# Optimization experiments

Measured on AMD Instinct MI355X. Metric: run time of the kernel, lower is better.

The kernel has to match this reference:

```python
import jax, jax.numpy as jnp
import numpy as np

N_HEAD, N_KV_HEAD, HEAD_DIM = 16, 4, 128
EPS = 1e-5


def rms_norm(x, eps=EPS):
    return x * jax.lax.rsqrt(jnp.mean(x * x, axis=-1, keepdims=True) + eps)


def apply_rope(x, cos, sin):
    # x: (B,T,H,D); cos/sin: (1,T,1,D//2)
    d = x.shape[-1] // 2
    x1, x2 = x[..., :d], x[..., d:]
    return jnp.concatenate([x1 * cos - x2 * sin, x1 * sin + x2 * cos], axis=-1)


def setup_inputs() -> dict:
    key = jax.random.key(0)
    ks = jax.random.split(key, 6)
    B, T, C = 4, 2048, 2048
    H, KV, D = N_HEAD, N_KV_HEAD, HEAD_DIM
    x = jax.random.normal(ks[0], (B, T, C), dtype=jnp.float32)
    # RoPE tables (llama-style, theta=10000)
    inv_freq = 1.0 / (10000.0 ** (jnp.arange(D // 2, dtype=jnp.float32) / (D // 2)))
    ang = jnp.arange(T, dtype=jnp.float32)[:, None] * inv_freq[None, :]  # (T, D/2)
    cos = jnp.cos(ang)[None, :, None, :]
    sin = jnp.sin(ang)[None, :, None, :]
    s = 0.02
    wq = jax.random.normal(ks[1], (C, H * D), dtype=jnp.float32) * s
    wk = jax.random.normal(ks[2], (C, KV * D), dtype=jnp.float32) * s
    wv = jax.random.normal(ks[3], (C, KV * D), dtype=jnp.float32) * s
    wproj = jax.random.normal(ks[4], (H * D, C), dtype=jnp.float32) * s
    return {"x": x, "cos": cos, "sin": sin, "wq": wq, "wk": wk, "wv": wv, "wproj": wproj}


def reference(x, cos, sin, wq, wk, wv, wproj):
    B, T, C = x.shape
    H, KV, D = N_HEAD, N_KV_HEAD, HEAD_DIM
    n_rep = H // KV
    q = (x @ wq).reshape(B, T, H, D)
    k = (x @ wk).reshape(B, T, KV, D)
    v = (x @ wv).reshape(B, T, KV, D)
    q = apply_rope(q, cos, sin)
    k = apply_rope(k, cos, sin)
    # QK-norm (use_qk_norm=True)
    q = rms_norm(q)
    k = rms_norm(k)
    # GQA: expand kv heads (matches torch repeat_interleave on head dim)
    k = jnp.repeat(k, n_rep, axis=2)
    v = jnp.repeat(v, n_rep, axis=2)
    scale = 1.0 / np.sqrt(D).astype(np.float32)
    scores = jnp.einsum('bqhd,bkhd->bhqk', q, k) * scale  # (B,H,T,T)
    causal = jnp.tril(jnp.ones((T, T), dtype=bool))
    scores = jnp.where(causal[None, None], scores, jnp.finfo(scores.dtype).min)
    p = jax.nn.softmax(scores, axis=-1)
    y = jnp.einsum('bhqk,bkhd->bqhd', p, v).reshape(B, T, H * D)
    return y @ wproj
```

## Files before the change

### kernel.cpp

```cpp
#include <hip/hip_runtime.h>
#include <hip/hip_bf16.h>
#include <stdint.h>

using bf16 = __hip_bfloat16;
typedef __attribute__((ext_vector_type(8))) short short8;
typedef __attribute__((ext_vector_type(4))) float f32x4;
typedef __attribute__((ext_vector_type(16))) float f32x16;

#define MFMA16(a,b,c) __builtin_amdgcn_mfma_f32_16x16x32_bf16(a,b,c,0,0,0)
#define MFMA32(a,b,c) __builtin_amdgcn_mfma_f32_32x32x16_bf16(a,b,c,0,0,0)

__device__ __forceinline__ void gload_lds16(const void* g, void* l) {
  __builtin_amdgcn_global_load_lds((const __attribute__((address_space(1))) void*)g,
                                   (__attribute__((address_space(3))) void*)l, 16, 0, 0);
}

__device__ __forceinline__ short bf_bits(float f) {
  bf16 h = __float2bfloat16(f);
  return *reinterpret_cast<short*>(&h);
}
__device__ __forceinline__ unsigned int pk2(float a, float b) {
  unsigned int r;
  asm("v_cvt_pk_bf16_f32 %0, %1, %2" : "=v"(r) : "v"(a), "v"(b));
  return r;
}
__device__ __forceinline__ float bf2f(short s) {
  return __uint_as_float((unsigned int)(unsigned short)s << 16);
}
__device__ __forceinline__ float exp2g(float x) { return __builtin_amdgcn_exp2f(x); }

__global__ __launch_bounds__(256) void f32_to_bf16_k(const float* __restrict__ in,
                                                     bf16* __restrict__ out, size_t n) {
  size_t i = ((size_t)blockIdx.x * 256 + threadIdx.x) * 8;
  if (i >= n) return;
  float4 a = *(const float4*)(in + i);
  float4 b = *(const float4*)(in + i + 4);
  short8 pk;
  pk[0] = bf_bits(a.x); pk[1] = bf_bits(a.y); pk[2] = bf_bits(a.z); pk[3] = bf_bits(a.w);
  pk[4] = bf_bits(b.x); pk[5] = bf_bits(b.y); pk[6] = bf_bits(b.z); pk[7] = bf_bits(b.w);
  *(short8*)(out + i) = pk;
}

__global__ __launch_bounds__(256) void transpose_cvt_k(const float* __restrict__ in,
                                                       bf16* __restrict__ out, int K, int N) {
  __shared__ float tile[32][33];
  int n0 = blockIdx.x * 32, k0 = blockIdx.y * 32;
  int tx = threadIdx.x & 31, ty = threadIdx.x >> 5;
#pragma unroll
  for (int j = 0; j < 4; ++j) {
    int kk = ty + j * 8;
    tile[kk][tx] = in[(size_t)(k0 + kk) * N + n0 + tx];
  }
  __syncthreads();
#pragma unroll
  for (int j = 0; j < 4; ++j) {
    int nn = ty + j * 8;
    out[(size_t)(n0 + nn) * K + k0 + tx] = __float2bfloat16(tile[tx][nn]);
  }
}

__global__ __launch_bounds__(256) void transpose_v_k(const bf16* __restrict__ qkv,
                                                     bf16* __restrict__ vt) {
  constexpr int T = 2048, Dh = 128, KV = 4, QKVW = 3072, VOFF = 2560;
  __shared__ bf16 tile[32][33];
  int t0 = blockIdx.x * 32, d0 = blockIdx.y * 32;
  int b = blockIdx.z >> 2, kv = blockIdx.z & 3;
  int tx = threadIdx.x & 31, ty = threadIdx.x >> 5;
#pragma unroll
  for (int j = 0; j < 4; ++j) {
    int tt = ty + j * 8;
    tile[tt][tx] = qkv[((size_t)(b * T + t0 + tt)) * QKVW + VOFF + kv * Dh + d0 + tx];
  }
  __syncthreads();
#pragma unroll
  for (int j = 0; j < 4; ++j) {
    int dd = ty + j * 8;
    vt[((size_t)((b * KV + kv) * Dh + d0 + dd)) * T + t0 + tx] = tile[tx][dd];
  }
}

__global__ __launch_bounds__(256) void rope_rms_k(bf16* __restrict__ buf, int rowstride,
                                                  int baseoff,
                                                  const float* __restrict__ cosp,
                                                  const float* __restrict__ sinp,
                                                  int nh, float outscale) {
  constexpr int T = 2048;
  int wid = blockIdx.x * 4 + (threadIdx.x >> 6);
  int lane = threadIdx.x & 63;
  int h = wid % nh;
  int tok = wid / nh;
  int t = tok & (T - 1);
  bf16* p = buf + (size_t)tok * rowstride + baseoff + h * 128;
  float x1 = __bfloat162float(p[lane]);
  float x2 = __bfloat162float(p[lane + 64]);
  float c = cosp[t * 64 + lane], s = sinp[t * 64 + lane];
  float o1 = x1 * c - x2 * s;
  float o2 = x1 * s + x2 * c;
  float ss = o1 * o1 + o2 * o2;
#pragma unroll
  for (int m = 1; m < 64; m <<= 1) ss += __shfl_xor(ss, m, 64);
  float r = rsqrtf(ss * (1.f / 128.f) + 1e-5f) * outscale;
  p[lane] = __float2bfloat16(o1 * r);
  p[lane + 64] = __float2bfloat16(o2 * r);
}

#define PHASE(buf, i0, ...)                                                       \
  {                                                                               \
    short8 a00 = ldA(buf, i0, 0), a01 = ldA(buf, i0, 1);                          \
    short8 a10 = ldA(buf, (i0) + 1, 0), a11 = ldA(buf, (i0) + 1, 1);              \
    __VA_ARGS__;                                                                  \
    __builtin_amdgcn_s_barrier();                                                 \
    asm volatile("s_waitcnt lgkmcnt(0)" ::: "memory");                            \
    __builtin_amdgcn_s_setprio(1);                                                \
    _Pragma("unroll") for (int j = 0; j < 4; ++j) {                               \
      acc[i0][j] = MFMA16(a00, bf_[2 * j], acc[i0][j]);                           \
      acc[i0][j] = MFMA16(a01, bf_[2 * j + 1], acc[i0][j]);                       \
      acc[(i0) + 1][j] = MFMA16(a10, bf_[2 * j], acc[(i0) + 1][j]);               \
      acc[(i0) + 1][j] = MFMA16(a11, bf_[2 * j + 1], acc[(i0) + 1][j]);           \
    }                                                                             \
    __builtin_amdgcn_s_setprio(0);                                                \
  }
#define LOADB(buf)                                                                \
  _Pragma("unroll") for (int j = 0; j < 4; ++j) {                                 \
    bf_[2 * j] = ldB(buf, j, 0);                                                  \
    bf_[2 * j + 1] = ldB(buf, j, 1);                                              \
  }
#define BAR __builtin_amdgcn_s_barrier()

template <typename OutT>
__global__ __launch_bounds__(512, 2) void gemm256(const bf16* __restrict__ A,
                                                  const bf16* __restrict__ Bt,
                                                  OutT* __restrict__ C, int K,
                                                  int NT, int ldC) {
  __shared__ char lds[131072];
  const int tid = threadIdx.x, lane = tid & 63, w = tid >> 6;
  const int wm = w >> 2, wn = w & 3;
  const int bx = blockIdx.x;
  const int chunk = gridDim.x >> 3;
  const int wgid = (bx & 7) * chunk + (bx >> 3);
  const int m0 = (wgid / NT) * 256, n0 = (wgid % NT) * 256;
  const int lm = lane & 15;
  const int sw = (lane & 7) << 4;
  const int g16 = (lane >> 4) << 4;
  const size_t strideAB = (size_t)K * 2;

  auto stageA = [&](int buf, int h, int t) {
#pragma unroll
    for (int p2 = 0; p2 < 2; ++p2) {
      int off = tid * 16 + p2 * 8192;
      int row = off >> 7, cb = off & 127;
      int scb = cb ^ ((row & 7) << 4);
      gload_lds16((const char*)A + (size_t)(m0 + h * 128 + row) * strideAB + t * 128 + scb,
                  lds + buf * 65536 + h * 16384 + off);
    }
  };
  auto stageB = [&](int buf, int h, int t) {
#pragma unroll
    for (int p2 = 0; p2 < 2; ++p2) {
      int off = tid * 16 + p2 * 8192;
      int row = off >> 7, cb = off & 127;
      int scb = cb ^ ((row & 7) << 4);
      gload_lds16((const char*)Bt + (size_t)(n0 + h * 128 + row) * strideAB + t * 128 + scb,
                  lds + buf * 65536 + 32768 + h * 16384 + off);
    }
  };
  auto ldA = [&](int buf, int i, int ks) {
    int row = wm * 128 + i * 16 + lm;
    return *(const short8*)(lds + buf * 65536 + row * 128 + ((ks * 64 + g16) ^ sw));
  };
  auto ldB = [&](int buf, int j, int ks) {
    int row = wn * 64 + j * 16 + lm;
    return *(const short8*)(lds + buf * 65536 + 32768 + row * 128 + ((ks * 64 + g16) ^ sw));
  };

  f32x4 acc[8][4] = {};
  short8 bf_[8];
  const int niter = K / 128;

  stageA(0, 0, 0); stageA(0, 1, 0); stageB(0, 0, 0); stageB(0, 1, 0);
  stageB(1, 0, 1); stageB(1, 1, 1);
  asm volatile("s_waitcnt vmcnt(4)" ::: "memory");
  BAR;

  for (int i = 0; i < niter; ++i) {
    const int t0 = 2 * i, t1 = 2 * i + 1;
    const bool nl = (i + 1 < niter);
    LOADB(0);
    PHASE(0, 0, stageA(1, 0, t1)); BAR;
    PHASE(0, 2, stageA(1, 1, t1)); BAR;
    PHASE(0, 4, if (nl) stageB(0, 0, t0 + 2)); BAR;
    PHASE(0, 6, if (nl) stageB(0, 1, t0 + 2));
    if (nl) { asm volatile("s_waitcnt vmcnt(4)" ::: "memory"); }
    else    { asm volatile("s_waitcnt vmcnt(0)" ::: "memory"); }
    BAR;
    LOADB(1);
    PHASE(1, 0, if (nl) stageA(0, 0, t0 + 2)); BAR;
    PHASE(1, 2, if (nl) stageA(0, 1, t0 + 2)); BAR;
    PHASE(1, 4, if (nl) stageB(1, 0, t1 + 2)); BAR;
    PHASE(1, 6, if (nl) stageB(1, 1, t1 + 2));
    if (nl) { asm volatile("s_waitcnt vmcnt(4)" ::: "memory"); }
    BAR;
  }

  if constexpr (sizeof(OutT) == 2) {
    __syncthreads();
    bf16* sC = (bf16*)lds;
#pragma unroll
    for (int i = 0; i < 8; ++i) {
      int row = wm * 128 + i * 16 + (lane >> 4) * 4;
#pragma unroll
      for (int j = 0; j < 4; ++j) {
        int col = wn * 64 + j * 16 + lm;
#pragma unroll
        for (int r = 0; r < 4; ++r) sC[(row + r) * 256 + col] = __float2bfloat16(acc[i][j][r]);
      }
    }
    __syncthreads();
#pragma unroll
    for (int p = 0; p < 16; ++p) {
      int off = tid * 16 + p * 8192;
      int row = off >> 9, cb = off & 511;
      *(short8*)((char*)C + ((size_t)(m0 + row) * ldC + n0) * 2 + cb) =
          *(const short8*)(lds + off);
    }
  } else {
#pragma unroll
    for (int i = 0; i < 8; ++i) {
      int row = m0 + wm * 128 + i * 16 + (lane >> 4) * 4;
#pragma unroll
      for (int j = 0; j < 4; ++j) {
        int col = n0 + wn * 64 + j * 16 + lm;
#pragma unroll
        for (int r = 0; r < 4; ++r) C[(size_t)(row + r) * ldC + col] = acc[i][j][r];
      }
    }
  }
}

template <typename OutT>
__global__ __launch_bounds__(256) void gemm_bt(const bf16* __restrict__ A,
                                               const bf16* __restrict__ Bt,
                                               OutT* __restrict__ C, int K,
                                               int NT, int ldC) {
  constexpr int BM = 128, BN = 128, BK = 64;
  __shared__ char smem[32768];
  bf16* sA = (bf16*)smem;
  bf16* sB = (bf16*)(smem + 16384);
  int tid = threadIdx.x;
  int lane = tid & 63, w = tid >> 6;
  int flat = blockIdx.x;
  int wgid = (flat & 7) * (gridDim.x >> 3) + (flat >> 3);
  int m0 = (wgid / NT) * BM, n0 = (wgid % NT) * BN;
  int wm = (w >> 1) * 64, wn = (w & 1) * 64;
  f32x4 acc[4][4] = {};
  int nk = K / BK;
  for (int kt = 0; kt < nk; ++kt) {
    __syncthreads();
    int kb = kt * BK;
#pragma unroll
    for (int it = 0; it < 4; ++it) {
      int off = tid * 16 + it * 4096;
      int row = off >> 7, cb = off & 127;
      gload_lds16((const char*)A + (((size_t)(m0 + row)) * K + kb) * 2 + cb, (char*)sA + off);
    }
#pragma unroll
    for (int it = 0; it < 4; ++it) {
      int off = tid * 16 + it * 4096;
      int row = off >> 7, cb = off & 127;
      gload_lds16((const char*)Bt + (((size_t)(n0 + row)) * K + kb) * 2 + cb, (char*)sB + off);
    }
    asm volatile("s_waitcnt vmcnt(0)" ::: "memory");
    __syncthreads();
#pragma unroll
    for (int ks = 0; ks < 2; ++ks) {
      short8 af[4], bfr[4];
#pragma unroll
      for (int i = 0; i < 4; ++i) {
        af[i]  = *(const short8*)(sA + (wm + i * 16 + (lane & 15)) * BK + ks * 32 + (lane >> 4) * 8);
        bfr[i] = *(const short8*)(sB + (wn + i * 16 + (lane & 15)) * BK + ks * 32 + (lane >> 4) * 8);
      }
#pragma unroll
      for (int i = 0; i < 4; ++i)
#pragma unroll
        for (int j = 0; j < 4; ++j)
          acc[i][j] = MFMA16(af[i], bfr[j], acc[i][j]);
    }
  }
  if constexpr (sizeof(OutT) == 2) {
    __syncthreads();
    bf16* sC = (bf16*)smem;
#pragma unroll
    for (int i = 0; i < 4; ++i) {
      int row = wm + i * 16 + (lane >> 4) * 4;
#pragma unroll
      for (int j = 0; j < 4; ++j) {
        int col = wn + j * 16 + (lane & 15);
#pragma unroll
        for (int r = 0; r < 4; ++r)
          sC[(row + r) * BN + col] = __float2bfloat16(acc[i][j][r]);
      }
    }
    __syncthreads();
#pragma unroll
    for (int it = 0; it < 8; ++it) {
      int off = tid * 16 + it * 4096;
      int row = off >> 8, cb = off & 255;
      *(short8*)((char*)C + ((size_t)(m0 + row) * ldC + n0) * 2 + cb) =
          *(const short8*)(smem + off);
    }
  } else {
#pragma unroll
    for (int i = 0; i < 4; ++i) {
      int row = m0 + wm + i * 16 + (lane >> 4) * 4;
#pragma unroll
      for (int j = 0; j < 4; ++j) {
        int col = n0 + wn + j * 16 + (lane & 15);
#pragma unroll
        for (int r = 0; r < 4; ++r)
          C[(size_t)(row + r) * ldC + col] = acc[i][j][r];
      }
    }
  }
}

__global__ __launch_bounds__(512, 2) void attn_k(const bf16* __restrict__ qkv,
                                                 const bf16* __restrict__ vt,
                                                 bf16* __restrict__ y,
                                                 const float* __restrict__ cosp,
                                                 const float* __restrict__ sinp) {
  constexpr int T = 2048, Dh = 128, KV = 4, KB = 64, QKVW = 3072, KOFF = 2048;
  __shared__ char lds[65536];
  const int tid = threadIdx.x, lane = tid & 63, w = tid >> 6;
  const int hi = lane >> 5, lq = lane & 31;
  const int bx = blockIdx.x;
  const int qt = 7 - (bx >> 6);
  const int b = (bx >> 4) & 3, h = bx & 15;
  const int kh = h >> 2;
  const int q0 = qt * 256 + w * 32;
  const int qg = q0 + lq;
  const int swz = (lane & 7) << 4;

  short8 aq[8];
  {
    const bf16* qp = qkv + ((size_t)(b * T + qg)) * QKVW + h * Dh + hi * 8;
#pragma unroll
    for (int m = 0; m < 8; ++m) aq[m] = *(const short8*)(qp + m * 16);
  }
  __builtin_amdgcn_s_waitcnt(0);

  {
    float ss = 0.f;
#pragma unroll
    for (int m = 0; m < 8; ++m)
#pragma unroll
      for (int e = 0; e < 8; ++e) { float v = bf2f(aq[m][e]); ss += v * v; }
    ss += __shfl_xor(ss, 32, 64);
    float rn = rsqrtf(ss * (1.f / 128.f) + 1e-5f) * (0.08838834764831845f * 1.4426950408889634f);
    const float4* cq4 = (const float4*)(cosp + (size_t)qg * 64) + hi * 2;
    const float4* sq4 = (const float4*)(sinp + (size_t)qg * 64) + hi * 2;
#pragma unroll
    for (int m = 0; m < 4; ++m) {
      float4 c0 = cq4[m * 4], c1 = cq4[m * 4 + 1];
      float4 s0 = sq4[m * 4], s1 = sq4[m * 4 + 1];
      float cc[8] = {c0.x, c0.y, c0.z, c0.w, c1.x, c1.y, c1.z, c1.w};
      float sn[8] = {s0.x, s0.y, s0.z, s0.w, s1.x, s1.y, s1.z, s1.w};
      short8 xl = aq[m], xh = aq[m + 4], nl, nh;
#pragma unroll
      for (int e = 0; e < 8; ++e) {
        float x1 = bf2f(xl[e]), x2 = bf2f(xh[e]);
        nl[e] = bf_bits((x1 * cc[e] - x2 * sn[e]) * rn);
        nh[e] = bf_bits((x1 * sn[e] + x2 * cc[e]) * rn);
      }
      aq[m] = nl; aq[m + 4] = nh;
    }
  }

  f32x16 acc[4] = {};
  float mrow = -1e4f, lrow = 0.f;

  auto stage = [&](int buf, int kv0) {
#pragma unroll
    for (int p = 0; p < 2; ++p) {
      int off = tid * 16 + p * 8192;
      int row = off >> 8, cb = off & 255;
      int scb = cb ^ ((row & 7) << 4);
      gload_lds16((const char*)qkv + (((size_t)(b * T + kv0 + row)) * QKVW + KOFF + kh * Dh) * 2 + scb,
                  lds + buf * 16384 + off);
    }
#pragma unroll
    for (int p = 0; p < 2; ++p) {
      int off = tid * 16 + p * 8192;
      int row = off >> 7, cb = off & 127;
      int scb = cb ^ ((row & 7) << 4);
      gload_lds16((const char*)vt + (((size_t)((b * KV + kh) * Dh + row)) * T + kv0) * 2 + scb,
                  lds + 32768 + buf * 16384 + off);
    }
  };

  const int nt = (qt + 1) * 4;
  const int lastit = (q0 + 31) >> 6;
  stage(0, 0);

  for (int it = 0; it < nt; ++it) {
    int cur = it & 1;
    if (it + 1 < nt) { stage(cur ^ 1, (it + 1) * KB); asm volatile("s_waitcnt vmcnt(4)" ::: "memory"); }
    else             { asm volatile("s_waitcnt vmcnt(0)" ::: "memory"); }
    __builtin_amdgcn_s_barrier();
    if (it <= lastit) {
      const char* sK = lds + cur * 16384;
      const char* sV = lds + 32768 + cur * 16384;
      const int kv0 = it * KB;

      f32x16 s0 = {}, s1 = {};
      __builtin_amdgcn_s_setprio(1);
#pragma unroll
      for (int m = 0; m < 8; ++m) {
        short8 ak = *(const short8*)(sK + lq * 256 + ((m * 32 + hi * 16) ^ swz));
        s0 = MFMA32(ak, aq[m], s0);
      }
#pragma unroll
      for (int m = 0; m < 8; ++m) {
        short8 ak = *(const short8*)(sK + (32 + lq) * 256 + ((m * 32 + hi * 16) ^ swz));
        s1 = MFMA32(ak, aq[m], s1);
      }
      __builtin_amdgcn_s_setprio(0);

      if (kv0 + 63 > q0) {
#pragma unroll
        for (int r = 0; r < 16; ++r) {
          int krow = (r & 3) + 8 * (r >> 2) + 4 * hi;
          if (kv0 + krow > qg) s0[r] = -1e30f;
          if (kv0 + 32 + krow > qg) s1[r] = -1e30f;
        }
      }

      float mx[16];
#pragma unroll
      for (int r = 0; r < 16; ++r) mx[r] = fmaxf(s0[r], s1[r]);
#pragma unroll
      for (int st = 8; st > 0; st >>= 1)
#pragma unroll
        for (int r = 0; r < 16; ++r) if (r < st) mx[r] = fmaxf(mx[r], mx[r + st]);
      float tmax = fmaxf(mx[0], __shfl_xor(mx[0], 32, 64));
      if (!__all(tmax - mrow <= 11.5f)) {
        float mn = fmaxf(mrow, tmax);
        float corr = exp2g(mrow - mn);
        mrow = mn;
        lrow *= corr;
#pragma unroll
        for (int dt = 0; dt < 4; ++dt)
#pragma unroll
          for (int r = 0; r < 16; ++r) acc[dt][r] *= corr;
      }
      float sm[16];
#pragma unroll
      for (int r = 0; r < 16; ++r) {
        s0[r] = exp2g(s0[r] - mrow);
        s1[r] = exp2g(s1[r] - mrow);
        sm[r] = s0[r] + s1[r];
      }
#pragma unroll
      for (int st = 8; st > 0; st >>= 1)
#pragma unroll
        for (int r = 0; r < 16; ++r) if (r < st) sm[r] += sm[r + st];
      lrow += sm[0] + __shfl_xor(sm[0], 32, 64);

      unsigned int u[16];
#pragma unroll
      for (int g = 0; g < 4; ++g) {
        u[g * 2 + 0] = pk2(s0[4 * g + 0], s0[4 * g + 1]);
        u[g * 2 + 1] = pk2(s0[4 * g + 2], s0[4 * g + 3]);
        u[8 + g * 2 + 0] = pk2(s1[4 * g + 0], s1[4 * g + 1]);
        u[8 + g * 2 + 1] = pk2(s1[4 * g + 2], s1[4 * g + 3]);
      }
      short8 pb[4];
#pragma unroll
      for (int kvs = 0; kvs < 4; ++kvs) {
        unsigned int lo0 = u[4 * kvs + 0], lo1 = u[4 * kvs + 1];
        unsigned int hi0 = u[4 * kvs + 2], hi1 = u[4 * kvs + 3];
        asm volatile("v_permlane32_swap_b32 %0, %1" : "+v"(lo0), "+v"(hi0));
        asm volatile("v_permlane32_swap_b32 %0, %1" : "+v"(lo1), "+v"(hi1));
        union { short8 v; unsigned int q[4]; } P;
        P.q[0] = lo0; P.q[1] = lo1; P.q[2] = hi0; P.q[3] = hi1;
        pb[kvs] = P.v;
      }

      __builtin_amdgcn_s_setprio(1);
#pragma unroll
      for (int dt = 0; dt < 4; ++dt) {
#pragma unroll
        for (int kvs = 0; kvs < 4; ++kvs) {
          short8 av = *(const short8*)(sV + (dt * 32 + lq) * 128 + ((kvs * 32 + hi * 16) ^ swz));
          acc[dt] = MFMA32(av, pb[kvs], acc[dt]);
        }
      }
      __builtin_amdgcn_s_setprio(0);
    }
    __builtin_amdgcn_s_barrier();
  }

  float inv = 1.f / lrow;
  __syncthreads();
  char* myO = lds + w * 8192;
#pragma unroll
  for (int dt = 0; dt < 4; ++dt)
#pragma unroll
    for (int i = 0; i < 8; ++i) {
      int d = ((2 * i) & 3) + 8 * (i >> 1) + 4 * hi;
      unsigned int pkd = pk2(acc[dt][2 * i] * inv, acc[dt][2 * i + 1] * inv);
      *(unsigned int*)(myO + lq * 256 + ((dt * 64 + d * 2) ^ ((lq & 7) << 4))) = pkd;
    }
  __syncthreads();
  const int row0 = b * T + qt * 256;
#pragma unroll
  for (int p = 0; p < 8; ++p) {
    int off = (p * 512 + tid) * 16;
    int q = off >> 8, cb = off & 255;
    short8 v = *(const short8*)(lds + (q >> 5) * 8192 + (q & 31) * 256 + (cb ^ ((q & 7) << 4)));
    *(short8*)((char*)y + ((size_t)(row0 + q) * 2048 + h * 128) * 2 + cb) = v;
  }
}

extern "C" void kernel_launch(void* const* d_in, const int* in_sizes, int n_in,
                              void* d_out, int out_size, void* d_ws, size_t ws_size,
                              hipStream_t stream) {
  const float* x    = (const float*)d_in[0];
  const float* cosp = (const float*)d_in[1];
  const float* sinp = (const float*)d_in[2];
  const float* wq   = (const float*)d_in[3];
  const float* wk   = (const float*)d_in[4];
  const float* wv   = (const float*)d_in[5];
  const float* wp   = (const float*)d_in[6];
  float* out = (float*)d_out;

  constexpr size_t Mtok = 8192;
  constexpr int Cdim = 2048, HD = 2048, KVD = 512, QKVW = 3072;

  char* ws = (char*)d_ws;
  bf16* xb    = (bf16*)ws; ws += Mtok * Cdim * 2;
  bf16* wqkvT = (bf16*)ws; ws += (size_t)QKVW * Cdim * 2;
  bf16* wpT   = (bf16*)ws; ws += (size_t)Cdim * HD * 2;
  bf16* qkv   = (bf16*)ws; ws += Mtok * QKVW * 2;
  bf16* vtb   = (bf16*)ws; ws += Mtok * KVD * 2;
  bf16* yb    = (bf16*)ws; ws += Mtok * HD * 2;

  f32_to_bf16_k<<<dim3(Mtok * Cdim / 8 / 256), 256, 0, stream>>>(x, xb, Mtok * Cdim);
  transpose_cvt_k<<<dim3(HD / 32, Cdim / 32), 256, 0, stream>>>(wq, wqkvT, Cdim, HD);
  transpose_cvt_k<<<dim3(KVD / 32, Cdim / 32), 256, 0, stream>>>(wk, wqkvT + (size_t)2048 * Cdim, Cdim, KVD);
  transpose_cvt_k<<<dim3(KVD / 32, Cdim / 32), 256, 0, stream>>>(wv, wqkvT + (size_t)2560 * Cdim, Cdim, KVD);
  transpose_cvt_k<<<dim3(Cdim / 32, HD / 32), 256, 0, stream>>>(wp, wpT, HD, Cdim);

  gemm256<bf16><<<dim3(256), 512, 0, stream>>>(xb, wqkvT, qkv, Cdim, 8, QKVW);
  gemm_bt<bf16><<<dim3(512), 256, 0, stream>>>(xb, wqkvT + (size_t)2048 * Cdim,
                                               (bf16*)qkv + 2048, Cdim, 8, QKVW);

  rope_rms_k<<<dim3(Mtok * 4 / 4), 256, 0, stream>>>(qkv, QKVW, 2048, cosp, sinp, 4, 1.0f);
  transpose_v_k<<<dim3(64, 4, 16), 256, 0, stream>>>(qkv, vtb);

  attn_k<<<dim3(512), 512, 0, stream>>>(qkv, vtb, yb, cosp, sinp);

  gemm256<float><<<dim3(256), 512, 0, stream>>>(yb, wpT, out, Cdim, 8, 2048);
}
```

Measured before the change: 316.0 us.

## Fuse K RoPE/RMS-norm and V transpose into KV GEMM epilogue; restructure attention prefetch

The KV projection GEMM becomes a dedicated kernel whose epilogue applies RoPE and RMS-norm to the K tiles in LDS and writes V tiles transposed straight into the vtb buffer. This removes the separate rope_rms_k and transpose_v_k launches and their global memory round trips. Separately, the attention loop now waits for all loads and then issues the next-tile prefetch after the barrier, dropping the trailing barrier. That trades the partial vmcnt wait for a simpler double-buffer schedule, which may expose more load latency.

```diff
diff --git a/kernel.cpp b/kernel.cpp
--- a/kernel.cpp
+++ b/kernel.cpp
@@ -57,51 +57,6 @@
     int nn = ty + j * 8;
     out[(size_t)(n0 + nn) * K + k0 + tx] = __float2bfloat16(tile[tx][nn]);
   }
-}
-
-__global__ __launch_bounds__(256) void transpose_v_k(const bf16* __restrict__ qkv,
-                                                     bf16* __restrict__ vt) {
-  constexpr int T = 2048, Dh = 128, KV = 4, QKVW = 3072, VOFF = 2560;
-  __shared__ bf16 tile[32][33];
-  int t0 = blockIdx.x * 32, d0 = blockIdx.y * 32;
-  int b = blockIdx.z >> 2, kv = blockIdx.z & 3;
-  int tx = threadIdx.x & 31, ty = threadIdx.x >> 5;
-#pragma unroll
-  for (int j = 0; j < 4; ++j) {
-    int tt = ty + j * 8;
-    tile[tt][tx] = qkv[((size_t)(b * T + t0 + tt)) * QKVW + VOFF + kv * Dh + d0 + tx];
-  }
-  __syncthreads();
-#pragma unroll
-  for (int j = 0; j < 4; ++j) {
-    int dd = ty + j * 8;
-    vt[((size_t)((b * KV + kv) * Dh + d0 + dd)) * T + t0 + tx] = tile[tx][dd];
-  }
-}
-
-__global__ __launch_bounds__(256) void rope_rms_k(bf16* __restrict__ buf, int rowstride,
-                                                  int baseoff,
-                                                  const float* __restrict__ cosp,
-                                                  const float* __restrict__ sinp,
-                                                  int nh, float outscale) {
-  constexpr int T = 2048;
-  int wid = blockIdx.x * 4 + (threadIdx.x >> 6);
-  int lane = threadIdx.x & 63;
-  int h = wid % nh;
-  int tok = wid / nh;
-  int t = tok & (T - 1);
-  bf16* p = buf + (size_t)tok * rowstride + baseoff + h * 128;
-  float x1 = __bfloat162float(p[lane]);
-  float x2 = __bfloat162float(p[lane + 64]);
-  float c = cosp[t * 64 + lane], s = sinp[t * 64 + lane];
-  float o1 = x1 * c - x2 * s;
-  float o2 = x1 * s + x2 * c;
-  float ss = o1 * o1 + o2 * o2;
-#pragma unroll
-  for (int m = 1; m < 64; m <<= 1) ss += __shfl_xor(ss, m, 64);
-  float r = rsqrtf(ss * (1.f / 128.f) + 1e-5f) * outscale;
-  p[lane] = __float2bfloat16(o1 * r);
-  p[lane + 64] = __float2bfloat16(o2 * r);
 }
 
 #define PHASE(buf, i0, ...)                                                       \
@@ -237,24 +192,24 @@
   }
 }
 
-template <typename OutT>
-__global__ __launch_bounds__(256) void gemm_bt(const bf16* __restrict__ A,
+__global__ __launch_bounds__(256) void gemm_kv(const bf16* __restrict__ A,
                                                const bf16* __restrict__ Bt,
-                                               OutT* __restrict__ C, int K,
-                                               int NT, int ldC) {
-  constexpr int BM = 128, BN = 128, BK = 64;
-  __shared__ char smem[32768];
+                                               bf16* __restrict__ qkv,
+                                               bf16* __restrict__ vtb,
+                                               const float* __restrict__ cosp,
+                                               const float* __restrict__ sinp) {
+  constexpr int BM = 128, BN = 128, BK = 64, K = 2048, QKVW = 3072, T = 2048, SCP = 132;
+  __shared__ char smem[BM * SCP * 2];
   bf16* sA = (bf16*)smem;
   bf16* sB = (bf16*)(smem + 16384);
   int tid = threadIdx.x;
   int lane = tid & 63, w = tid >> 6;
   int flat = blockIdx.x;
   int wgid = (flat & 7) * (gridDim.x >> 3) + (flat >> 3);
-  int m0 = (wgid / NT) * BM, n0 = (wgid % NT) * BN;
+  int m0 = (wgid >> 3) * BM, n0 = (wgid & 7) * BN;
   int wm = (w >> 1) * 64, wn = (w & 1) * 64;
   f32x4 acc[4][4] = {};
-  int nk = K / BK;
-  for (int kt = 0; kt < nk; ++kt) {
+  for (int kt = 0; kt < K / BK; ++kt) {
     __syncthreads();
     int kb = kt * BK;
 #pragma unroll
@@ -286,9 +241,12 @@
           acc[i][j] = MFMA16(af[i], bfr[j], acc[i][j]);
     }
   }
-  if constexpr (sizeof(OutT) == 2) {
-    __syncthreads();
-    bf16* sC = (bf16*)smem;
+
+  const int kvh = (n0 >> 7) & 3;
+  const int b = m0 >> 11, t0 = m0 & (T - 1);
+  bf16* sC = (bf16*)smem;
+  __syncthreads();
+  if (n0 >= 512) {
 #pragma unroll
     for (int i = 0; i < 4; ++i) {
       int row = wm + i * 16 + (lane >> 4) * 4;
@@ -296,29 +254,51 @@
       for (int j = 0; j < 4; ++j) {
         int col = wn + j * 16 + (lane & 15);
 #pragma unroll
-        for (int r = 0; r < 4; ++r)
-          sC[(row + r) * BN + col] = __float2bfloat16(acc[i][j][r]);
-      }
-    }
-    __syncthreads();
-#pragma unroll
-    for (int it = 0; it < 8; ++it) {
-      int off = tid * 16 + it * 4096;
-      int row = off >> 8, cb = off & 255;
-      *(short8*)((char*)C + ((size_t)(m0 + row) * ldC + n0) * 2 + cb) =
-          *(const short8*)(smem + off);
+        for (int r = 0; r < 4; ++r) sC[col * SCP + row + r] = __float2bfloat16(acc[i][j][r]);
+      }
+    }
+    __syncthreads();
+#pragma unroll
+    for (int p = 0; p < 8; ++p) {
+      int g = p * 2048 + tid * 8;
+      int d = g >> 7, tb = g & 127;
+      *(short8*)(vtb + ((size_t)((b * 4 + kvh) * 128 + d)) * T + t0 + tb) =
+          *(const short8*)(sC + d * SCP + tb);
     }
   } else {
 #pragma unroll
     for (int i = 0; i < 4; ++i) {
-      int row = m0 + wm + i * 16 + (lane >> 4) * 4;
+      int row = wm + i * 16 + (lane >> 4) * 4;
 #pragma unroll
       for (int j = 0; j < 4; ++j) {
-        int col = n0 + wn + j * 16 + (lane & 15);
-#pragma unroll
-        for (int r = 0; r < 4; ++r)
-          C[(size_t)(row + r) * ldC + col] = acc[i][j][r];
-      }
+        int col = wn + j * 16 + (lane & 15);
+#pragma unroll
+        for (int r = 0; r < 4; ++r) sC[(row + r) * SCP + col] = __float2bfloat16(acc[i][j][r]);
+      }
+    }
+    __syncthreads();
+    for (int rr = 0; rr < 32; ++rr) {
+      int row = w * 32 + rr;
+      int t = t0 + row;
+      float x1 = __bfloat162float(sC[row * SCP + lane]);
+      float x2 = __bfloat162float(sC[row * SCP + lane + 64]);
+      float c = cosp[t * 64 + lane], s = sinp[t * 64 + lane];
+      float o1 = x1 * c - x2 * s;
+      float o2 = x1 * s + x2 * c;
+      float ss = o1 * o1 + o2 * o2;
+#pragma unroll
+      for (int m = 1; m < 64; m <<= 1) ss += __shfl_xor(ss, m, 64);
+      float r = rsqrtf(ss * (1.f / 128.f) + 1e-5f);
+      sC[row * SCP + lane] = __float2bfloat16(o1 * r);
+      sC[row * SCP + lane + 64] = __float2bfloat16(o2 * r);
+    }
+    __syncthreads();
+#pragma unroll
+    for (int p = 0; p < 8; ++p) {
+      int g = p * 2048 + tid * 8;
+      int row = g >> 7, cb = g & 127;
+      *(short8*)(qkv + (size_t)(m0 + row) * QKVW + 2048 + kvh * 128 + cb) =
+          *(const short8*)(sC + row * SCP + cb);
     }
   }
 }
@@ -400,12 +380,12 @@
   const int nt = (qt + 1) * 4;
   const int lastit = (q0 + 31) >> 6;
   stage(0, 0);
+  int cur = 0;
 
   for (int it = 0; it < nt; ++it) {
-    int cur = it & 1;
-    if (it + 1 < nt) { stage(cur ^ 1, (it + 1) * KB); asm volatile("s_waitcnt vmcnt(4)" ::: "memory"); }
-    else             { asm volatile("s_waitcnt vmcnt(0)" ::: "memory"); }
+    asm volatile("s_waitcnt vmcnt(0)" ::: "memory");
     __builtin_amdgcn_s_barrier();
+    if (it + 1 < nt) stage(cur ^ 1, (it + 1) * KB);
     if (it <= lastit) {
       const char* sK = lds + cur * 16384;
       const char* sV = lds + 32768 + cur * 16384;
@@ -496,7 +476,7 @@
       }
       __builtin_amdgcn_s_setprio(0);
     }
-    __builtin_amdgcn_s_barrier();
+    cur ^= 1;
   }
 
   float inv = 1.f / lrow;
@@ -551,11 +531,7 @@
   transpose_cvt_k<<<dim3(Cdim / 32, HD / 32), 256, 0, stream>>>(wp, wpT, HD, Cdim);
 
   gemm256<bf16><<<dim3(256), 512, 0, stream>>>(xb, wqkvT, qkv, Cdim, 8, QKVW);
-  gemm_bt<bf16><<<dim3(512), 256, 0, stream>>>(xb, wqkvT + (size_t)2048 * Cdim,
-                                               (bf16*)qkv + 2048, Cdim, 8, QKVW);
-
-  rope_rms_k<<<dim3(Mtok * 4 / 4), 256, 0, stream>>>(qkv, QKVW, 2048, cosp, sinp, 4, 1.0f);
-  transpose_v_k<<<dim3(64, 4, 16), 256, 0, stream>>>(qkv, vtb);
+  gemm_kv<<<dim3(512), 256, 0, stream>>>(xb, wqkvT + (size_t)2048 * Cdim, qkv, vtb, cosp, sinp);
 
   attn_k<<<dim3(512), 512, 0, stream>>>(qkv, vtb, yb, cosp, sinp);
 
```

Result: no change. 315.3 us (median of 2 runs) (-0.2%).
